# Optimization experiments

Hardware: AMD Instinct MI355X
Metric: run time of the kernel (lower is better)

The kernel has to match this reference:

```python
import jax, jax.numpy as jnp
import numpy as np

B, T, D, H = 4, 4096, 256, 64  # batch, seq, DIM_EMBEDDING (fixed constant), head_size


def setup_inputs() -> dict:
    key = jax.random.key(0)
    ks = jax.random.split(key, 6)
    x = jax.random.normal(ks[0], (B, T, D), dtype=jnp.float32)
    scale = jnp.float32(0.02)
    Wq = jax.random.normal(ks[1], (D, H), dtype=jnp.float32) * scale
    Wk = jax.random.normal(ks[2], (D, H), dtype=jnp.float32) * scale
    Wv = jax.random.normal(ks[3], (D, H), dtype=jnp.float32) * scale
    two_pi = jnp.float32(2.0 * np.pi)
    angles_x = jax.random.uniform(ks[4], (T, H // 4), dtype=jnp.float32, maxval=two_pi)
    angles_y = jax.random.uniform(ks[5], (T, H // 4), dtype=jnp.float32, maxval=two_pi)
    return {"x": x, "Wq": Wq, "Wk": Wk, "Wv": Wv, "angles_x": angles_x, "angles_y": angles_y}


def _rope_half(v, freqs):
    # v: (B, T, H/2) real; freqs: (T, H/4) complex64 (unit phasors)
    b, t, h = v.shape
    vc = v.astype(jnp.float32).reshape(b, t, h // 2, 2)
    vz = jax.lax.complex(vc[..., 0], vc[..., 1])         # (B, T, H/4)
    rz = vz * freqs[None]                                 # complex multiply per position
    out = jnp.stack([jnp.real(rz), jnp.imag(rz)], axis=-1)
    return out.reshape(b, t, h)


def _rope2d(v, fx, fy):
    vx, vy = jnp.split(v, 2, axis=-1)
    return jnp.concatenate([_rope_half(vx, fx), _rope_half(vy, fy)], axis=-1)


def reference(x, Wq, Wk, Wv, angles_x, angles_y):
    # complex unit phasors e^{i*theta}
    fx = jax.lax.complex(jnp.cos(angles_x), jnp.sin(angles_x))
    fy = jax.lax.complex(jnp.cos(angles_y), jnp.sin(angles_y))
    # original apply_rotary_embeddings is wrapped in @torch.no_grad -> detached
    q = jax.lax.stop_gradient(_rope2d(x @ Wq, fx, fy))
    k = jax.lax.stop_gradient(_rope2d(x @ Wk, fx, fy))
    v = x @ Wv
    C = x.shape[-1]  # NOTE: source scales by embedding dim (256), not head dim
    wei = jnp.einsum('bth,bsh->bts', q, k) / jnp.sqrt(jnp.float32(C))
    softwei = jax.nn.softmax(wei, axis=-1)  # no causal mask in source
    out = jnp.einsum('bts,bsh->bth', softwei, v)
    return out
```

## Files before the change

kernel.cpp:

```cpp
#include <hip/hip_runtime.h>

#define B_ 4
#define T_ 4096
#define D_ 256
#define H_ 64
#define NBT (B_ * T_)
#define NBTH (B_ * T_ * H_)

typedef __bf16 bf16x8 __attribute__((ext_vector_type(8)));
typedef float f32x4 __attribute__((ext_vector_type(4)));

__device__ __forceinline__ unsigned short f2bf(float f) {
  union { float f; unsigned int u; } v; v.f = f;
  unsigned int u = v.u;
  return (unsigned short)((u + 0x7fffu + ((u >> 16) & 1u)) >> 16);
}

#if __has_builtin(__builtin_amdgcn_cvt_pk_bf16_f32)
typedef __bf16 bf16x2_t __attribute__((ext_vector_type(2)));
__device__ __forceinline__ unsigned int pk2(float a, float b) {
  union { bf16x2_t v; unsigned int u; } c;
  c.v = __builtin_amdgcn_cvt_pk_bf16_f32(a, b);
  return c.u;
}
#else
__device__ __forceinline__ unsigned int pk2(float a, float b) {
  return (unsigned int)f2bf(a) | ((unsigned int)f2bf(b) << 16);
}
#endif

#if __has_builtin(__builtin_amdgcn_exp2f)
#define EXP2(x) __builtin_amdgcn_exp2f(x)
#else
#define EXP2(x) exp2f(x)
#endif

#define QSCALE 0.09016844f


__global__ __launch_bounds__(256) void prep_w_kernel(
    const float* __restrict__ Wq, const float* __restrict__ Wk,
    const float* __restrict__ Wv, unsigned short* __restrict__ wt) {
  const int m = blockIdx.x;
  const float* W = (m == 0) ? Wq : (m == 1) ? Wk : Wv;
  const float scale = (m == 0) ? QSCALE : 1.f;
  __shared__ unsigned short tile[64][264];
  int h = threadIdx.x & 63, dq = threadIdx.x >> 6;
  for (int d = dq; d < D_; d += 4)
    tile[h][d] = f2bf(W[d * H_ + h] * scale);
  __syncthreads();
  int ht = threadIdx.x >> 6;
  int lane = threadIdx.x & 63, quad = lane >> 4, l16 = lane & 15;
#pragma unroll
  for (int c = 0; c < 8; ++c) {
    bf16x8 v = *(const bf16x8*)&tile[ht * 16 + l16][c * 32 + quad * 8];
    *(bf16x8*)&wt[(((m * 4 + ht) * 8 + c) << 9) + lane * 8] = v;
  }
}

__global__ __launch_bounds__(192) void qkv_kernel(
    const float* __restrict__ x, const unsigned short* __restrict__ wt,
    const float* __restrict__ axg, const float* __restrict__ ayg,
    unsigned short* __restrict__ qo, unsigned short* __restrict__ ko,
    unsigned short* __restrict__ vt) {
  const int row0g = blockIdx.x * 16;
  const int tid = threadIdx.x;
  const int w = tid / 64, lane = tid & 63, quad = lane >> 4, l16 = lane & 15;

  __shared__ unsigned short xs[16][264];
  __shared__ unsigned short qkt[2][16][72];
  __shared__ unsigned short vsh[64][16];

  const float4* xb = (const float4*)(x + (size_t)row0g * D_);
  for (int i = tid; i < 1024; i += 192) {
    float4 v = xb[i];
    int r = i >> 6, c4 = (i & 63) << 2;
    *(unsigned int*)&xs[r][c4] = pk2(v.x, v.y);
    *(unsigned int*)&xs[r][c4 + 2] = pk2(v.z, v.w);
  }
  __syncthreads();

  bf16x8 xf[8];
#pragma unroll
  for (int c = 0; c < 8; ++c)
    xf[c] = *(const bf16x8*)&xs[l16][c * 32 + quad * 8];

  const unsigned short* wb = wt + (((size_t)w * 4) * 8 << 9);
  f32x4 acc[4];
#pragma unroll
  for (int ht = 0; ht < 4; ++ht) acc[ht] = (f32x4){0.f, 0.f, 0.f, 0.f};
#pragma unroll
  for (int c = 0; c < 8; ++c) {
#pragma unroll
    for (int ht = 0; ht < 4; ++ht) {
      bf16x8 wf = *(const bf16x8*)&wb[((ht * 8 + c) << 9) + lane * 8];
      acc[ht] = __builtin_amdgcn_mfma_f32_16x16x32_bf16(xf[c], wf, acc[ht],
                                                        0, 0, 0);
    }
  }

  const int row0loc = row0g & (T_ - 1);
  if (w < 2) {
    const float sgn = (l16 & 1) ? 1.f : -1.f;
#pragma unroll
    for (int ht = 0; ht < 4; ++ht) {
      int hh = ht * 16 + l16;
      int pidx = (hh & 31) >> 1;
      const float* ab = (hh >= 32) ? ayg : axg;
#pragma unroll
      for (int r = 0; r < 4; ++r) {
        int t = row0loc + quad * 4 + r;
        float s, c;
        __sincosf(ab[t * 16 + pidx], &s, &c);
        float val = acc[ht][r];
        float par = __shfl_xor(val, 1);
        qkt[w][quad * 4 + r][hh] = f2bf(val * c + sgn * par * s);
      }
    }
    asm volatile("s_waitcnt lgkmcnt(0)" ::: "memory");
    unsigned short* dst;
    size_t base;
    if (w == 0) {
      dst = qo;
      base = ((size_t)(row0g >> 4) * 2) << 9;
    } else {
      dst = ko;
      base = ((size_t)((row0g >> 6) * 8 + ((row0g >> 4) & 3) * 2)) << 9;
    }
#pragma unroll
    for (int half = 0; half < 2; ++half) {
      bf16x8 v = *(const bf16x8*)&qkt[w][l16][half * 32 + quad * 8];
      *(bf16x8*)&dst[base + half * 512 + lane * 8] = v;
    }
  } else {
#pragma unroll
    for (int ht = 0; ht < 4; ++ht)
#pragma unroll
      for (int r = 0; r < 4; ++r)
        vsh[ht * 16 + l16][quad * 4 + r] = f2bf(acc[ht][r]);
    asm volatile("s_waitcnt lgkmcnt(0)" ::: "memory");
    const int kvblk = row0g >> 6;
    const int mt = (row0g >> 4) & 3;
    const int half_v = mt >> 1, qlow = (mt & 1) * 2;
#pragma unroll
    for (int it = 0; it < 2; ++it) {
      int hhx = it * 2 + (quad >> 1);
      int qp = qlow + (quad & 1);
      bf16x8 v = *(const bf16x8*)&vsh[hhx * 16 + l16][(quad & 1) * 8];
      *(bf16x8*)&vt[((((size_t)kvblk * 4 + hhx) * 2 + half_v) << 9) +
                    (qp * 16 + l16) * 8] = v;
    }
  }
}

#define LDP 72

__global__ __launch_bounds__(256, 4) void attn_kernel(
    const unsigned short* __restrict__ qfg, const unsigned short* __restrict__ kfg,
    const unsigned short* __restrict__ vfg, float* __restrict__ opart,
    float* __restrict__ lpart, int kv_len) {
  const int split = blockIdx.x >> 7;
  const int rem = blockIdx.x & 127;
  const int b = rem >> 5;
  const int q0 = (rem & 31) * 128;
  const int tid = threadIdx.x;
  const int w = tid >> 6, lane = tid & 63, quad = lane >> 4, l16 = lane & 15;

  __shared__ unsigned short Ps[4][32 * LDP];

  bf16x8 qf[2][2];
#pragma unroll
  for (int u = 0; u < 2; ++u) {
    size_t rb = (size_t)(b * T_ + q0 + w * 32 + u * 16) >> 4;
#pragma unroll
    for (int half = 0; half < 2; ++half)
      qf[u][half] = *(const bf16x8*)&qfg[((rb * 2 + half) << 9) + lane * 8];
  }

  f32x4 oacc[2][4];
  float lsum[2] = {0.f, 0.f};
  const f32x4 vzero = {0.f, 0.f, 0.f, 0.f};
#pragma unroll
  for (int u = 0; u < 2; ++u)
#pragma unroll
    for (int hh = 0; hh < 4; ++hh) oacc[u][hh] = vzero;

  const int kvb0 = (b * T_ + split * kv_len) >> 6;
  const int nkvb = kv_len >> 6;
  const int rot = rem & (nkvb - 1);

  for (int i = 0; i < nkvb; ++i) {
    const int kb = (i + rot) & (nkvb - 1);
    const unsigned short* kfb = kfg + ((size_t)(kvb0 + kb) << 12);
    const unsigned short* vfb = vfg + ((size_t)(kvb0 + kb) << 12);

#pragma unroll
    for (int mt = 0; mt < 4; ++mt) {
      bf16x8 k0 = *(const bf16x8*)&kfb[((mt * 2 + 0) << 9) + lane * 8];
      bf16x8 k1 = *(const bf16x8*)&kfb[((mt * 2 + 1) << 9) + lane * 8];
#pragma unroll
      for (int u = 0; u < 2; ++u) {
        f32x4 s = vzero;
        s = __builtin_amdgcn_mfma_f32_16x16x32_bf16(k0, qf[u][0], s, 0, 0, 0);
        s = __builtin_amdgcn_mfma_f32_16x16x32_bf16(k1, qf[u][1], s, 0, 0, 0);
        float p0 = EXP2(s[0]);
        float p1 = EXP2(s[1]);
        float p2 = EXP2(s[2]);
        float p3 = EXP2(s[3]);
        lsum[u] += (p0 + p1) + (p2 + p3);
        uint2 pk;
        pk.x = pk2(p0, p1);
        pk.y = pk2(p2, p3);
        *(uint2*)&Ps[w][(u * 16 + l16) * LDP + mt * 16 + quad * 4] = pk;
      }
    }
    asm volatile("s_waitcnt lgkmcnt(0)" ::: "memory");

#pragma unroll
    for (int hh = 0; hh < 4; ++hh) {
      bf16x8 v0 = *(const bf16x8*)&vfb[((hh * 2 + 0) << 9) + lane * 8];
      bf16x8 v1 = *(const bf16x8*)&vfb[((hh * 2 + 1) << 9) + lane * 8];
#pragma unroll
      for (int u = 0; u < 2; ++u) {
        bf16x8 ap0 =
            *(const bf16x8*)&Ps[w][(u * 16 + l16) * LDP + quad * 8];
        bf16x8 ap1 =
            *(const bf16x8*)&Ps[w][(u * 16 + l16) * LDP + 32 + quad * 8];
        oacc[u][hh] =
            __builtin_amdgcn_mfma_f32_16x16x32_bf16(ap0, v0, oacc[u][hh], 0, 0, 0);
        oacc[u][hh] =
            __builtin_amdgcn_mfma_f32_16x16x32_bf16(ap1, v1, oacc[u][hh], 0, 0, 0);
      }
    }
  }

#pragma unroll
  for (int u = 0; u < 2; ++u) {
    lsum[u] += __shfl_xor(lsum[u], 16);
    lsum[u] += __shfl_xor(lsum[u], 32);
    size_t base = (size_t)(split * B_ + b) * T_ + q0 + w * 32 + u * 16;
    if (quad == 0) lpart[base + l16] = lsum[u];
#pragma unroll
    for (int r = 0; r < 4; ++r) {
      float* orow = opart + (base + quad * 4 + r) * H_;
#pragma unroll
      for (int hh = 0; hh < 4; ++hh) orow[hh * 16 + l16] = oacc[u][hh][r];
    }
  }
}

__global__ __launch_bounds__(256) void combine_kernel(
    const float* __restrict__ opart, const float* __restrict__ lpart,
    float* __restrict__ out, int ns) {
  int idx = blockIdx.x * 256 + threadIdx.x;
  int bt = idx >> 4;
  float den = 0.f;
  float axx = 0.f, ayy = 0.f, azz = 0.f, aww = 0.f;
  for (int s = 0; s < ns; ++s) {
    den += lpart[s * NBT + bt];
    float4 o = ((const float4*)opart)[(size_t)s * (NBTH / 4) + idx];
    axx += o.x; ayy += o.y; azz += o.z; aww += o.w;
  }
  float inv = 1.f / den;
  float4 res;
  res.x = axx * inv; res.y = ayy * inv; res.z = azz * inv; res.w = aww * inv;
  ((float4*)out)[idx] = res;
}

extern "C" void kernel_launch(void* const* d_in, const int* in_sizes, int n_in,
                              void* d_out, int out_size, void* d_ws,
                              size_t ws_size, hipStream_t stream) {
  const float* x  = (const float*)d_in[0];
  const float* Wq = (const float*)d_in[1];
  const float* Wk = (const float*)d_in[2];
  const float* Wv = (const float*)d_in[3];
  const float* ax = (const float*)d_in[4];
  const float* ay = (const float*)d_in[5];
  float* out = (float*)d_out;

  unsigned short* qo = (unsigned short*)d_ws;
  unsigned short* ko = qo + NBTH;
  unsigned short* vt = ko + NBTH;
  unsigned short* wt = vt + NBTH;
  float* opart = (float*)(wt + 3 * H_ * D_);

  size_t fixed = (size_t)3 * NBTH * 2 + (size_t)3 * H_ * D_ * 2;
  int NS = (ws_size >= fixed + (size_t)8 * NBTH * 4 + (size_t)8 * NBT * 4 + 256)
               ? 8 : 4;
  float* lpart = opart + (size_t)NS * NBTH;

  prep_w_kernel<<<3, 256, 0, stream>>>(Wq, Wk, Wv, wt);
  qkv_kernel<<<NBT / 16, 192, 0, stream>>>(x, wt, ax, ay, qo, ko, vt);
  attn_kernel<<<NS * 128, 256, 0, stream>>>(qo, ko, vt, opart, lpart, T_ / NS);
  combine_kernel<<<NBTH / 4 / 256, 256, 0, stream>>>(opart, lpart, out, NS);
}
```

Measured before the change: 118.7 us.

## Reduce split-KV partials with atomic adds into output instead of combine pass

Each KV-split block now atomically adds its unnormalized output tile straight into the zeroed output buffer. A light normalize kernel then divides by the summed per-split denominators. This removes the large per-split partial output buffer and the combine kernel's reads of it. The cost is an extra memset, fp32 atomic contention at L2, and a non-deterministic summation order. The split count is fixed at 8 and the per-block KV rotation is dropped.

```diff
diff --git a/kernel.cpp b/kernel.cpp
--- a/kernel.cpp
+++ b/kernel.cpp
@@ -4,6 +4,7 @@
 #define T_ 4096
 #define D_ 256
 #define H_ 64
+#define NS 8
 #define NBT (B_ * T_)
 #define NBTH (B_ * T_ * H_)
 
@@ -157,8 +158,8 @@
 
 __global__ __launch_bounds__(256, 4) void attn_kernel(
     const unsigned short* __restrict__ qfg, const unsigned short* __restrict__ kfg,
-    const unsigned short* __restrict__ vfg, float* __restrict__ opart,
-    float* __restrict__ lpart, int kv_len) {
+    const unsigned short* __restrict__ vfg, float* __restrict__ outacc,
+    float* __restrict__ lpart) {
   const int split = blockIdx.x >> 7;
   const int rem = blockIdx.x & 127;
   const int b = rem >> 5;
@@ -185,12 +186,11 @@
 #pragma unroll
     for (int hh = 0; hh < 4; ++hh) oacc[u][hh] = vzero;
 
+  const int kv_len = T_ / NS;
   const int kvb0 = (b * T_ + split * kv_len) >> 6;
   const int nkvb = kv_len >> 6;
-  const int rot = rem & (nkvb - 1);
-
-  for (int i = 0; i < nkvb; ++i) {
-    const int kb = (i + rot) & (nkvb - 1);
+
+  for (int kb = 0; kb < nkvb; ++kb) {
     const unsigned short* kfb = kfg + ((size_t)(kvb0 + kb) << 12);
     const unsigned short* vfb = vfg + ((size_t)(kvb0 + kb) << 12);
 
@@ -238,33 +238,29 @@
   for (int u = 0; u < 2; ++u) {
     lsum[u] += __shfl_xor(lsum[u], 16);
     lsum[u] += __shfl_xor(lsum[u], 32);
-    size_t base = (size_t)(split * B_ + b) * T_ + q0 + w * 32 + u * 16;
-    if (quad == 0) lpart[base + l16] = lsum[u];
+    size_t row = (size_t)b * T_ + q0 + w * 32 + u * 16;
+    if (quad == 0) lpart[(size_t)split * NBT + row + l16] = lsum[u];
 #pragma unroll
     for (int r = 0; r < 4; ++r) {
-      float* orow = opart + (base + quad * 4 + r) * H_;
-#pragma unroll
-      for (int hh = 0; hh < 4; ++hh) orow[hh * 16 + l16] = oacc[u][hh][r];
-    }
-  }
-}
-
-__global__ __launch_bounds__(256) void combine_kernel(
-    const float* __restrict__ opart, const float* __restrict__ lpart,
-    float* __restrict__ out, int ns) {
+      float* orow = outacc + (row + quad * 4 + r) * H_;
+#pragma unroll
+      for (int hh = 0; hh < 4; ++hh)
+        atomicAdd(&orow[hh * 16 + l16], oacc[u][hh][r]);
+    }
+  }
+}
+
+__global__ __launch_bounds__(256) void normalize_kernel(
+    const float* __restrict__ lpart, float* __restrict__ out) {
   int idx = blockIdx.x * 256 + threadIdx.x;
   int bt = idx >> 4;
   float den = 0.f;
-  float axx = 0.f, ayy = 0.f, azz = 0.f, aww = 0.f;
-  for (int s = 0; s < ns; ++s) {
-    den += lpart[s * NBT + bt];
-    float4 o = ((const float4*)opart)[(size_t)s * (NBTH / 4) + idx];
-    axx += o.x; ayy += o.y; azz += o.z; aww += o.w;
-  }
+#pragma unroll
+  for (int s = 0; s < NS; ++s) den += lpart[(size_t)s * NBT + bt];
   float inv = 1.f / den;
-  float4 res;
-  res.x = axx * inv; res.y = ayy * inv; res.z = azz * inv; res.w = aww * inv;
-  ((float4*)out)[idx] = res;
+  float4 o = ((const float4*)out)[idx];
+  o.x *= inv; o.y *= inv; o.z *= inv; o.w *= inv;
+  ((float4*)out)[idx] = o;
 }
 
 extern "C" void kernel_launch(void* const* d_in, const int* in_sizes, int n_in,
@@ -282,15 +278,12 @@
   unsigned short* ko = qo + NBTH;
   unsigned short* vt = ko + NBTH;
   unsigned short* wt = vt + NBTH;
-  float* opart = (float*)(wt + 3 * H_ * D_);
-
-  size_t fixed = (size_t)3 * NBTH * 2 + (size_t)3 * H_ * D_ * 2;
-  int NS = (ws_size >= fixed + (size_t)8 * NBTH * 4 + (size_t)8 * NBT * 4 + 256)
-               ? 8 : 4;
-  float* lpart = opart + (size_t)NS * NBTH;
+  float* lpart = (float*)(wt + 3 * H_ * D_);
+
+  hipMemsetAsync(d_out, 0, (size_t)out_size * sizeof(float), stream);
 
   prep_w_kernel<<<3, 256, 0, stream>>>(Wq, Wk, Wv, wt);
   qkv_kernel<<<NBT / 16, 192, 0, stream>>>(x, wt, ax, ay, qo, ko, vt);
-  attn_kernel<<<NS * 128, 256, 0, stream>>>(qo, ko, vt, opart, lpart, T_ / NS);
-  combine_kernel<<<NBTH / 4 / 256, 256, 0, stream>>>(opart, lpart, out, NS);
-}
+  attn_kernel<<<NS * 128, 256, 0, stream>>>(qo, ko, vt, out, lpart);
+  normalize_kernel<<<NBTH / 4 / 256, 256, 0, stream>>>(lpart, out);
+}
```

Measured after the change: 134.9 us. 1.14x slower.

## Double per-wave query rows in attention to reuse K/V loads across more rows

Applied to the files above, without the earlier changes.

Each attention block now covers 256 query rows (64 per wave) instead of 128, so every K/V fragment loaded from global memory feeds twice as many MFMAs. The grid halves to NS*64 blocks and launch bounds drop to 2 waves-per-EU occupancy to make room for the larger accumulator and register footprint. The P fragments are hoisted out of the V loop, the KV rotation offset is removed, and NS is fixed at 8 at compile time, which also lets the combine loop unroll. Risks are higher register pressure, lower occupancy, fewer blocks to fill the CUs, and dropping the workspace-size check that used to pick NS.

```diff
diff --git a/kernel.cpp b/kernel.cpp
--- a/kernel.cpp
+++ b/kernel.cpp
@@ -4,6 +4,7 @@
 #define T_ 4096
 #define D_ 256
 #define H_ 64
+#define NS 8
 #define NBT (B_ * T_)
 #define NBTH (B_ * T_ * H_)
 
@@ -155,42 +156,41 @@
 
 #define LDP 72
 
-__global__ __launch_bounds__(256, 4) void attn_kernel(
+__global__ __launch_bounds__(256, 2) void attn_kernel(
     const unsigned short* __restrict__ qfg, const unsigned short* __restrict__ kfg,
     const unsigned short* __restrict__ vfg, float* __restrict__ opart,
-    float* __restrict__ lpart, int kv_len) {
-  const int split = blockIdx.x >> 7;
-  const int rem = blockIdx.x & 127;
-  const int b = rem >> 5;
-  const int q0 = (rem & 31) * 128;
+    float* __restrict__ lpart) {
+  const int split = blockIdx.x >> 6;
+  const int rem = blockIdx.x & 63;
+  const int b = rem >> 4;
+  const int q0 = (rem & 15) * 256;
   const int tid = threadIdx.x;
   const int w = tid >> 6, lane = tid & 63, quad = lane >> 4, l16 = lane & 15;
 
-  __shared__ unsigned short Ps[4][32 * LDP];
-
-  bf16x8 qf[2][2];
-#pragma unroll
-  for (int u = 0; u < 2; ++u) {
-    size_t rb = (size_t)(b * T_ + q0 + w * 32 + u * 16) >> 4;
+  __shared__ unsigned short Ps[4][64 * LDP];
+
+  bf16x8 qf[4][2];
+#pragma unroll
+  for (int u = 0; u < 4; ++u) {
+    size_t rb = (size_t)(b * T_ + q0 + w * 64 + u * 16) >> 4;
 #pragma unroll
     for (int half = 0; half < 2; ++half)
       qf[u][half] = *(const bf16x8*)&qfg[((rb * 2 + half) << 9) + lane * 8];
   }
 
-  f32x4 oacc[2][4];
-  float lsum[2] = {0.f, 0.f};
+  f32x4 oacc[4][4];
+  float lsum[4] = {0.f, 0.f, 0.f, 0.f};
   const f32x4 vzero = {0.f, 0.f, 0.f, 0.f};
 #pragma unroll
-  for (int u = 0; u < 2; ++u)
+  for (int u = 0; u < 4; ++u)
 #pragma unroll
     for (int hh = 0; hh < 4; ++hh) oacc[u][hh] = vzero;
 
+  const int kv_len = T_ / NS;
   const int kvb0 = (b * T_ + split * kv_len) >> 6;
   const int nkvb = kv_len >> 6;
-  const int rot = rem & (nkvb - 1);
-
-  for (int i = 0; i < nkvb; ++i) {
-    const int kb = (i + rot) & (nkvb - 1);
+
+  for (int kb = 0; kb < nkvb; ++kb) {
     const unsigned short* kfb = kfg + ((size_t)(kvb0 + kb) << 12);
     const unsigned short* vfb = vfg + ((size_t)(kvb0 + kb) << 12);
 
@@ -199,7 +199,7 @@
       bf16x8 k0 = *(const bf16x8*)&kfb[((mt * 2 + 0) << 9) + lane * 8];
       bf16x8 k1 = *(const bf16x8*)&kfb[((mt * 2 + 1) << 9) + lane * 8];
 #pragma unroll
-      for (int u = 0; u < 2; ++u) {
+      for (int u = 0; u < 4; ++u) {
         f32x4 s = vzero;
         s = __builtin_amdgcn_mfma_f32_16x16x32_bf16(k0, qf[u][0], s, 0, 0, 0);
         s = __builtin_amdgcn_mfma_f32_16x16x32_bf16(k1, qf[u][1], s, 0, 0, 0);
@@ -216,29 +216,33 @@
     }
     asm volatile("s_waitcnt lgkmcnt(0)" ::: "memory");
 
+    bf16x8 ap[4][2];
+#pragma unroll
+    for (int u = 0; u < 4; ++u)
+#pragma unroll
+      for (int half = 0; half < 2; ++half)
+        ap[u][half] = *(const bf16x8*)&Ps[w][(u * 16 + l16) * LDP +
+                                             half * 32 + quad * 8];
+
 #pragma unroll
     for (int hh = 0; hh < 4; ++hh) {
       bf16x8 v0 = *(const bf16x8*)&vfb[((hh * 2 + 0) << 9) + lane * 8];
       bf16x8 v1 = *(const bf16x8*)&vfb[((hh * 2 + 1) << 9) + lane * 8];
 #pragma unroll
-      for (int u = 0; u < 2; ++u) {
-        bf16x8 ap0 =
-            *(const bf16x8*)&Ps[w][(u * 16 + l16) * LDP + quad * 8];
-        bf16x8 ap1 =
-            *(const bf16x8*)&Ps[w][(u * 16 + l16) * LDP + 32 + quad * 8];
+      for (int u = 0; u < 4; ++u) {
         oacc[u][hh] =
-            __builtin_amdgcn_mfma_f32_16x16x32_bf16(ap0, v0, oacc[u][hh], 0, 0, 0);
+            __builtin_amdgcn_mfma_f32_16x16x32_bf16(ap[u][0], v0, oacc[u][hh], 0, 0, 0);
         oacc[u][hh] =
-            __builtin_amdgcn_mfma_f32_16x16x32_bf16(ap1, v1, oacc[u][hh], 0, 0, 0);
+            __builtin_amdgcn_mfma_f32_16x16x32_bf16(ap[u][1], v1, oacc[u][hh], 0, 0, 0);
       }
     }
   }
 
 #pragma unroll
-  for (int u = 0; u < 2; ++u) {
+  for (int u = 0; u < 4; ++u) {
     lsum[u] += __shfl_xor(lsum[u], 16);
     lsum[u] += __shfl_xor(lsum[u], 32);
-    size_t base = (size_t)(split * B_ + b) * T_ + q0 + w * 32 + u * 16;
+    size_t base = (size_t)(split * B_ + b) * T_ + q0 + w * 64 + u * 16;
     if (quad == 0) lpart[base + l16] = lsum[u];
 #pragma unroll
     for (int r = 0; r < 4; ++r) {
@@ -251,13 +255,14 @@
 
 __global__ __launch_bounds__(256) void combine_kernel(
     const float* __restrict__ opart, const float* __restrict__ lpart,
-    float* __restrict__ out, int ns) {
+    float* __restrict__ out) {
   int idx = blockIdx.x * 256 + threadIdx.x;
   int bt = idx >> 4;
   float den = 0.f;
   float axx = 0.f, ayy = 0.f, azz = 0.f, aww = 0.f;
-  for (int s = 0; s < ns; ++s) {
-    den += lpart[s * NBT + bt];
+#pragma unroll
+  for (int s = 0; s < NS; ++s) {
+    den += lpart[(size_t)s * NBT + bt];
     float4 o = ((const float4*)opart)[(size_t)s * (NBTH / 4) + idx];
     axx += o.x; ayy += o.y; azz += o.z; aww += o.w;
   }
@@ -283,14 +288,10 @@
   unsigned short* vt = ko + NBTH;
   unsigned short* wt = vt + NBTH;
   float* opart = (float*)(wt + 3 * H_ * D_);
-
-  size_t fixed = (size_t)3 * NBTH * 2 + (size_t)3 * H_ * D_ * 2;
-  int NS = (ws_size >= fixed + (size_t)8 * NBTH * 4 + (size_t)8 * NBT * 4 + 256)
-               ? 8 : 4;
   float* lpart = opart + (size_t)NS * NBTH;
 
   prep_w_kernel<<<3, 256, 0, stream>>>(Wq, Wk, Wv, wt);
   qkv_kernel<<<NBT / 16, 192, 0, stream>>>(x, wt, ax, ay, qo, ko, vt);
-  attn_kernel<<<NS * 128, 256, 0, stream>>>(qo, ko, vt, opart, lpart, T_ / NS);
-  combine_kernel<<<NBTH / 4 / 256, 256, 0, stream>>>(opart, lpart, out, NS);
-}
+  attn_kernel<<<NS * 64, 256, 0, stream>>>(qo, ko, vt, opart, lpart);
+  combine_kernel<<<NBTH / 4 / 256, 256, 0, stream>>>(opart, lpart, out);
+}
```

Measured after the change: 122.3 us. 3.0% more time.
